# Kernel tuning notes

Measured on AMD Instinct MI355X. Metric: run time of the kernel, lower is better.

## Reference

```python
import jax, jax.numpy as jnp
import numpy as np

NUM_HEADS = 8
MODEL_DIM = 1024
SEQ_LEN = 2048


def setup_inputs() -> dict:
    key = jax.random.key(0)
    ks = jax.random.split(key, 9)
    H, D, L = NUM_HEADS, MODEL_DIM, SEQ_LEN
    s_in = 1.0 / np.sqrt(D)
    s_out = 1.0 / np.sqrt(H * D)
    return {
        "tokens": jax.random.normal(ks[0], (D, L), dtype=jnp.float32),
        "Wq": jax.random.uniform(ks[1], (H * D, D), jnp.float32, -s_in, s_in),
        "bq": jax.random.uniform(ks[2], (H * D,), jnp.float32, -s_in, s_in),
        "Wk": jax.random.uniform(ks[3], (H * D, D), jnp.float32, -s_in, s_in),
        "bk": jax.random.uniform(ks[4], (H * D,), jnp.float32, -s_in, s_in),
        "Wv": jax.random.uniform(ks[5], (H * D, D), jnp.float32, -s_in, s_in),
        "bv": jax.random.uniform(ks[6], (H * D,), jnp.float32, -s_in, s_in),
        "Wo": jax.random.uniform(ks[7], (D, H * D), jnp.float32, -s_out, s_out),
        "bo": jax.random.uniform(ks[8], (D,), jnp.float32, -s_out, s_out),
    }


def _split_heads(x, H, D, L):
    # Faithful to torch: raw .view of contiguous [H*D, L] into (L, H, D),
    # then permute(1, 2, 0) -> (H, D, L). This is a memory reinterpretation,
    # not a transpose, exactly as in the original module.
    return x.reshape(L, H, D).transpose(1, 2, 0)


def reference(tokens, Wq, bq, Wk, bk, Wv, bv, Wo, bo):
    D, L = tokens.shape
    H = Wq.shape[0] // D
    # 1x1 Conv1d == matmul over channel dim
    q = _split_heads(Wq @ tokens + bq[:, None], H, D, L)  # (H, D, L)
    k = _split_heads(Wk @ tokens + bk[:, None], H, D, L)  # (H, D, L)
    v = _split_heads(Wv @ tokens + bv[:, None], H, D, L)  # (H, D, L)
    scores = jnp.einsum("hdl,hdm->hlm", q, k) / np.sqrt(D)  # (H, L, L)
    # torch F.softmax without dim on a 3D tensor -> dim=0 (head axis)
    attn = jax.nn.softmax(scores, axis=0)
    ctx = jnp.einsum("hlm,hdm->hdl", attn, v)  # (H, D, L)
    out = Wo @ ctx.reshape(H * D, L) + bo[:, None]  # (D, L)
    return out
```

## Files before the change

### kernel.cpp

```cpp
#include <hip/hip_runtime.h>

#define SEQL 2048
#define DMODEL 1024
#define HDIM 8192

typedef unsigned short bf16_t;
typedef __attribute__((ext_vector_type(8))) short bf16x8;
typedef __attribute__((ext_vector_type(4))) float f32x4;

__device__ __forceinline__ bf16_t f2bf(float f) {
  unsigned u = __float_as_uint(f);
  u += 0x7fffu + ((u >> 16) & 1u);
  return (bf16_t)(u >> 16);
}
__device__ __forceinline__ float bf2f(bf16_t b) {
  return __uint_as_float(((unsigned)b) << 16);
}

__global__ __launch_bounds__(256) void cvt_f32_bf16(const float* __restrict__ in,
                                                    bf16_t* __restrict__ out, int n) {
  int i = (blockIdx.x * 256 + threadIdx.x) * 4;
  if (i >= n) return;
  float4 f = *reinterpret_cast<const float4*>(in + i);
  ushort4 u;
  u.x = f2bf(f.x); u.y = f2bf(f.y); u.z = f2bf(f.z); u.w = f2bf(f.w);
  *reinterpret_cast<ushort4*>(out + i) = u;
}

__global__ __launch_bounds__(256) void cvt3_f32_bf16(const float* __restrict__ a,
                                                     const float* __restrict__ b,
                                                     const float* __restrict__ c,
                                                     bf16_t* __restrict__ out) {
  const int SEG = HDIM * DMODEL;
  int i = (blockIdx.x * 256 + threadIdx.x) * 4;
  const float* src;
  int off;
  if (i < SEG) { src = a; off = i; }
  else if (i < 2 * SEG) { src = b; off = i - SEG; }
  else { src = c; off = i - 2 * SEG; }
  float4 f = *reinterpret_cast<const float4*>(src + off);
  ushort4 u;
  u.x = f2bf(f.x); u.y = f2bf(f.y); u.z = f2bf(f.z); u.w = f2bf(f.w);
  *reinterpret_cast<ushort4*>(out + i) = u;
}

__global__ __launch_bounds__(256) void bias3(const float* __restrict__ a,
                                             const float* __restrict__ b,
                                             const float* __restrict__ c,
                                             float* __restrict__ out) {
  int i = blockIdx.x * 256 + threadIdx.x;
  float v = (i < HDIM) ? a[i] : (i < 2 * HDIM) ? b[i - HDIM] : c[i - 2 * HDIM];
  out[i] = v;
}

__global__ __launch_bounds__(256) void transpose_cvt(const float* __restrict__ in,
                                                     bf16_t* __restrict__ out) {
  __shared__ float tile[32][33];
  int bx = blockIdx.x * 32;
  int by = blockIdx.y * 32;
  int tx = threadIdx.x, ty = threadIdx.y;
#pragma unroll
  for (int i = ty; i < 32; i += 8)
    tile[i][tx] = in[(size_t)(by + i) * SEQL + bx + tx];
  __syncthreads();
#pragma unroll
  for (int i = ty; i < 32; i += 8)
    out[(size_t)(bx + i) * DMODEL + by + tx] = f2bf(tile[tx][i]);
}

__global__ __launch_bounds__(256) void softmax_heads(bf16_t* __restrict__ S) {
  const size_t HS = (size_t)SEQL * SEQL;
  size_t p = ((size_t)blockIdx.x * 256 + threadIdx.x) * 8;
  float v[8][8];
#pragma unroll
  for (int h = 0; h < 8; ++h) {
    bf16x8 x = *reinterpret_cast<const bf16x8*>(S + h * HS + p);
#pragma unroll
    for (int e = 0; e < 8; ++e) v[h][e] = bf2f((bf16_t)x[e]);
  }
#pragma unroll
  for (int e = 0; e < 8; ++e) {
    float mx = v[0][e];
#pragma unroll
    for (int h = 1; h < 8; ++h) mx = fmaxf(mx, v[h][e]);
    float s = 0.f;
#pragma unroll
    for (int h = 0; h < 8; ++h) { v[h][e] = __expf(v[h][e] - mx); s += v[h][e]; }
    float inv = 1.0f / s;
#pragma unroll
    for (int h = 0; h < 8; ++h) v[h][e] *= inv;
  }
#pragma unroll
  for (int h = 0; h < 8; ++h) {
    bf16x8 x;
#pragma unroll
    for (int e = 0; e < 8; ++e) x[e] = (short)f2bf(v[h][e]);
    *reinterpret_cast<bf16x8*>(S + h * HS + p) = x;
  }
}

__global__ __launch_bounds__(256) void reduce_out(const bf16_t* __restrict__ P,
                                                  const float* __restrict__ bo,
                                                  float* __restrict__ out) {
  const size_t NEL = (size_t)DMODEL * SEQL;
  size_t i = ((size_t)blockIdx.x * 256 + threadIdx.x) * 8;
  float s[8] = {0.f, 0.f, 0.f, 0.f, 0.f, 0.f, 0.f, 0.f};
#pragma unroll
  for (int z = 0; z < 8; ++z) {
    bf16x8 x = *reinterpret_cast<const bf16x8*>(P + z * NEL + i);
#pragma unroll
    for (int e = 0; e < 8; ++e) s[e] += bf2f((bf16_t)x[e]);
  }
  float bias = bo[i >> 11];
  float4 o0 = {s[0] + bias, s[1] + bias, s[2] + bias, s[3] + bias};
  float4 o1 = {s[4] + bias, s[5] + bias, s[6] + bias, s[7] + bias};
  *reinterpret_cast<float4*>(out + i) = o0;
  *reinterpret_cast<float4*>(out + i + 4) = o1;
}

template <int EPI, bool HAS_BIAS>
__global__ __launch_bounds__(512, 2) void gemm256(
    const bf16_t* __restrict__ A, const bf16_t* __restrict__ B,
    bf16_t* __restrict__ C, bf16_t* __restrict__ C2, const float* __restrict__ bias,
    int K, int lda, int ldb, int ldc,
    long long sA, long long sB, long long sC, float scale, int gx, int gxy) {
  __shared__ alignas(16) char smem[163840];
  auto* As = reinterpret_cast<bf16_t(*)[2][8192]>(smem);
  auto* Bs = reinterpret_cast<bf16_t(*)[2][8192]>(smem + 98304);
  const int nwg = gridDim.x;
  const int bid = blockIdx.x;
  const int swz = (nwg & 7) ? bid : ((bid & 7) * (nwg >> 3) + (bid >> 3));
  const int zz = swz / gxy;
  const int rem = swz - zz * gxy;
  const int brow = (rem / gx) * 256;
  const int bcol = (rem % gx) * 256;
  A += (long long)zz * sA;
  B += (long long)zz * sB;
  C += (long long)zz * sC;
  const int tid = threadIdx.x;
  const int w = tid >> 6, lane = tid & 63;
  const int fr = lane & 15, fq = lane >> 4;
  const int wr = w >> 2, wc = w & 3;

  int rj[2], cj[2];
#pragma unroll
  for (int j = 0; j < 2; ++j) {
    const int c = (w * 2 + j) * 64 + lane;
    rj[j] = c >> 3;
    cj[j] = ((c & 7) ^ (rj[j] & 7)) << 3;
  }

  auto stageA = [&](int buf, int kk) {
#pragma unroll
    for (int half = 0; half < 2; ++half)
#pragma unroll
      for (int j = 0; j < 2; ++j) {
        const bf16_t* g = A + (size_t)(brow + half * 128 + rj[j]) * lda + kk + cj[j];
        __builtin_amdgcn_global_load_lds(
            (const __attribute__((address_space(1))) void*)g,
            (__attribute__((address_space(3))) void*)(&As[buf][half][(w * 2 + j) * 512]),
            16, 0, 0);
      }
  };
  auto stageB = [&](int buf, int kk) {
#pragma unroll
    for (int half = 0; half < 2; ++half)
#pragma unroll
      for (int j = 0; j < 2; ++j) {
        const bf16_t* g = B + (size_t)(bcol + half * 128 + rj[j]) * ldb + kk + cj[j];
        __builtin_amdgcn_global_load_lds(
            (const __attribute__((address_space(1))) void*)g,
            (__attribute__((address_space(3))) void*)(&Bs[buf][half][(w * 2 + j) * 512]),
            16, 0, 0);
      }
  };

  auto ldA = [&](int buf, int mf, int kk) -> bf16x8 {
    const int rr = mf * 16 + fr;
    return *reinterpret_cast<const bf16x8*>(
        &As[buf][wr][rr * 64 + ((((kk << 2) | fq) ^ (rr & 7)) << 3)]);
  };
  auto ldB = [&](int buf, int nf, int kk) -> bf16x8 {
    const int rr = (wc & 1) * 64 + nf * 16 + fr;
    return *reinterpret_cast<const bf16x8*>(
        &Bs[buf][wc >> 1][rr * 64 + ((((kk << 2) | fq) ^ (rr & 7)) << 3)]);
  };

  f32x4 acc[8][4];
  const f32x4 fzero = {0.f, 0.f, 0.f, 0.f};
#pragma unroll
  for (int m = 0; m < 8; ++m)
#pragma unroll
    for (int n = 0; n < 4; ++n) acc[m][n] = fzero;

  const int NT = K >> 6;

  stageA(0, 0);
  stageB(0, 0);
  stageA(1, 64);
  asm volatile("s_waitcnt vmcnt(4)" ::: "memory");
  __builtin_amdgcn_sched_barrier(0);
  __builtin_amdgcn_s_barrier();
  __builtin_amdgcn_sched_barrier(0);

  int pa = 0;
  for (int t = 0; t < NT; ++t) {
    const int pb = t & 1;
    const bool pre1 = (t + 1 < NT), pre2 = (t + 2 < NT);
    int sa = pa + 2; if (sa >= 3) sa -= 3;
    bf16x8 af[4][2], bg[4][2];

    if (pre1) stageB(pb ^ 1, (t + 1) << 6);
#pragma unroll
    for (int mf = 0; mf < 4; ++mf)
#pragma unroll
      for (int kk = 0; kk < 2; ++kk) af[mf][kk] = ldA(pa, mf, kk);
#pragma unroll
    for (int nf = 0; nf < 2; ++nf)
#pragma unroll
      for (int kk = 0; kk < 2; ++kk) bg[nf][kk] = ldB(pb, nf, kk);
    __builtin_amdgcn_s_setprio(1);
#pragma unroll
    for (int mf = 0; mf < 4; ++mf)
#pragma unroll
      for (int nf = 0; nf < 2; ++nf)
#pragma unroll
        for (int kk = 0; kk < 2; ++kk)
          acc[mf][nf] = __builtin_amdgcn_mfma_f32_16x16x32_bf16(
              af[mf][kk], bg[nf][kk], acc[mf][nf], 0, 0, 0);
    __builtin_amdgcn_s_setprio(0);

    if (pre2) stageA(sa, (t + 2) << 6);
#pragma unroll
    for (int nf = 2; nf < 4; ++nf)
#pragma unroll
      for (int kk = 0; kk < 2; ++kk) bg[nf][kk] = ldB(pb, nf, kk);
    __builtin_amdgcn_s_setprio(1);
#pragma unroll
    for (int mf = 0; mf < 4; ++mf)
#pragma unroll
      for (int nf = 2; nf < 4; ++nf)
#pragma unroll
        for (int kk = 0; kk < 2; ++kk)
          acc[mf][nf] = __builtin_amdgcn_mfma_f32_16x16x32_bf16(
              af[mf][kk], bg[nf][kk], acc[mf][nf], 0, 0, 0);
    __builtin_amdgcn_s_setprio(0);

#pragma unroll
    for (int mf = 0; mf < 4; ++mf)
#pragma unroll
      for (int kk = 0; kk < 2; ++kk) af[mf][kk] = ldA(pa, mf + 4, kk);
    __builtin_amdgcn_s_setprio(1);
#pragma unroll
    for (int mf = 0; mf < 4; ++mf)
#pragma unroll
      for (int nf = 2; nf < 4; ++nf)
#pragma unroll
        for (int kk = 0; kk < 2; ++kk)
          acc[mf + 4][nf] = __builtin_amdgcn_mfma_f32_16x16x32_bf16(
              af[mf][kk], bg[nf][kk], acc[mf + 4][nf], 0, 0, 0);
    __builtin_amdgcn_s_setprio(0);

#pragma unroll
    for (int nf = 0; nf < 2; ++nf)
#pragma unroll
      for (int kk = 0; kk < 2; ++kk) bg[nf][kk] = ldB(pb, nf, kk);
    __builtin_amdgcn_s_setprio(1);
#pragma unroll
    for (int mf = 0; mf < 4; ++mf)
#pragma unroll
      for (int nf = 0; nf < 2; ++nf)
#pragma unroll
        for (int kk = 0; kk < 2; ++kk)
          acc[mf + 4][nf] = __builtin_amdgcn_mfma_f32_16x16x32_bf16(
              af[mf][kk], bg[nf][kk], acc[mf + 4][nf], 0, 0, 0);
    __builtin_amdgcn_s_setprio(0);

    if (pre1) {
      __builtin_amdgcn_sched_barrier(0);
      if (pre2) {
        asm volatile("s_waitcnt vmcnt(4)" ::: "memory");
      } else {
        asm volatile("s_waitcnt vmcnt(0)" ::: "memory");
      }
      __builtin_amdgcn_sched_barrier(0);
      __builtin_amdgcn_s_barrier();
      __builtin_amdgcn_sched_barrier(0);
    }
    ++pa; if (pa >= 3) pa = 0;
  }

  __syncthreads();

  const bool vseg = (EPI == 2) && (brow >= 2 * HDIM);
  if ((EPI == 0) || ((EPI == 2) && !vseg)) {
    bf16_t* Ct = (bf16_t*)smem;
#pragma unroll
    for (int mf = 0; mf < 8; ++mf)
#pragma unroll
      for (int j = 0; j < 4; ++j) {
        const int orow = wr * 128 + mf * 16 + fq * 4 + j;
        float bvv = HAS_BIAS ? bias[brow + orow] : 0.f;
#pragma unroll
        for (int nf = 0; nf < 4; ++nf)
          Ct[orow * 264 + wc * 64 + nf * 16 + fr] = f2bf(acc[mf][nf][j] * scale + bvv);
      }
    __syncthreads();
#pragma unroll
    for (int i = 0; i < 16; ++i) {
      const int c = tid + i * 512;
      const int row = c >> 5, ch = c & 31;
      *reinterpret_cast<bf16x8*>(&C[(size_t)(brow + row) * ldc + bcol + ch * 8]) =
          *reinterpret_cast<const bf16x8*>(smem + row * 528 + ch * 16);
    }
  } else if constexpr (EPI == 2) {
    const int vrow = brow - 2 * HDIM;
    bf16_t* Vt = (bf16_t*)smem;
#pragma unroll
    for (int mf = 0; mf < 8; ++mf)
#pragma unroll
      for (int j = 0; j < 4; ++j) {
        const int i = wr * 128 + mf * 16 + fq * 4 + j;
        const int mloc = i >> 2;
        float bvv = HAS_BIAS ? bias[brow + i] : 0.f;
#pragma unroll
        for (int nf = 0; nf < 4; ++nf) {
          const int dloc = wc * 64 + nf * 16 + fr;
          Vt[(j * 256 + dloc) * 72 + mloc] = f2bf(acc[mf][nf][j] * scale + bvv);
        }
      }
    __syncthreads();
    const int r_ = bcol >> 10, d0 = bcol & 1023, m0 = vrow >> 2;
#pragma unroll
    for (int sIt = 0; sIt < 2; ++sIt) {
      const int s = tid + sIt * 512;
      const int h2 = s >> 8, dloc = s & 255;
      const bf16_t* src = Vt + (h2 * 256 + dloc) * 72;
      bf16_t* dst = C2 + ((size_t)(2 * h2 + r_) * DMODEL + d0 + dloc) * SEQL + m0;
#pragma unroll
      for (int qq = 0; qq < 8; ++qq)
        *reinterpret_cast<bf16x8*>(dst + qq * 8) =
            *reinterpret_cast<const bf16x8*>(src + qq * 8);
    }
  }
}

extern "C" void kernel_launch(void* const* d_in, const int* in_sizes, int n_in,
                              void* d_out, int out_size, void* d_ws, size_t ws_size,
                              hipStream_t stream) {
  const float* tokens = (const float*)d_in[0];
  const float* Wq = (const float*)d_in[1];
  const float* bq = (const float*)d_in[2];
  const float* Wk = (const float*)d_in[3];
  const float* bk = (const float*)d_in[4];
  const float* Wv = (const float*)d_in[5];
  const float* bv = (const float*)d_in[6];
  const float* Wo = (const float*)d_in[7];
  const float* bo = (const float*)d_in[8];
  float* out = (float*)d_out;
  char* ws = (char*)d_ws;
  const size_t MB = 1024ull * 1024ull;
  bf16_t* Vs = (bf16_t*)(ws + 0);
  bf16_t* QmKm = (bf16_t*)(ws + 32 * MB);
  bf16_t* Qm = QmKm;
  bf16_t* Km = QmKm + (size_t)HDIM * SEQL;
  bf16_t* Sb = (bf16_t*)(ws + 96 * MB);
  bf16_t* tT = (bf16_t*)(ws + 96 * MB);
  bf16_t* Wqkv = (bf16_t*)(ws + 100 * MB);
  float* bqkv = (float*)(ws + 148 * MB);
  bf16_t* cT = (bf16_t*)(ws + 32 * MB);
  bf16_t* Wob = (bf16_t*)(ws + 64 * MB);
  bf16_t* Pp = (bf16_t*)(ws + 96 * MB);

  dim3 b256(256);
  dim3 b512(512);
  const int nW = HDIM * DMODEL;

  transpose_cvt<<<dim3(SEQL / 32, DMODEL / 32), dim3(32, 8), 0, stream>>>(tokens, tT);
  cvt3_f32_bf16<<<3 * nW / 1024, b256, 0, stream>>>(Wq, Wk, Wv, Wqkv);
  bias3<<<3 * HDIM / 256, b256, 0, stream>>>(bq, bk, bv, bqkv);

  gemm256<2, true><<<dim3(768, 1, 1), b512, 0, stream>>>(
      Wqkv, tT, QmKm, Vs, bqkv, DMODEL, DMODEL, DMODEL, SEQL,
      0, 0, 0, 1.0f, 8, 768);

  gemm256<0, false><<<dim3(512, 1, 1), b512, 0, stream>>>(
      Qm, Km, Sb, nullptr, nullptr, DMODEL, HDIM, HDIM, SEQL,
      1024, 1024, (long long)SEQL * SEQL, 0.03125f, 8, 64);

  softmax_heads<<<(SEQL * SEQL / 8) / 256, b256, 0, stream>>>(Sb);

  gemm256<0, false><<<dim3(256, 1, 1), b512, 0, stream>>>(
      Sb, Vs, cT, nullptr, nullptr, SEQL, SEQL, SEQL, HDIM,
      (long long)SEQL * SEQL, (long long)DMODEL * SEQL, 1024, 1.0f, 4, 32);

  cvt_f32_bf16<<<nW / 1024, b256, 0, stream>>>(Wo, Wob, nW);
  gemm256<0, false><<<dim3(256, 1, 1), b512, 0, stream>>>(
      Wob, cT, Pp, nullptr, nullptr, 1024, HDIM, HDIM, SEQL,
      1024, 1024, (long long)DMODEL * SEQL, 1.0f, 8, 32);
  reduce_out<<<(DMODEL * SEQL / 8) / 256, b256, 0, stream>>>(Pp, bo, out);
}
```

Measured before the change: 357.9 us.

## Double-buffer A in GEMM main loop with per-phase barriers; hoist Wo conversion

The GEMM main loop drops the triple-buffered A tiles for double buffering, which shrinks LDS from 160 KB to 144 KB. Each MFMA phase is now wrapped in block barriers plus an lgkmcnt wait, and the A prefetch for tile t+2 moves to the last phase so it can safely overwrite the current buffer. The Wo fp32-to-bf16 conversion is launched at the start, with a new workspace location so it no longer aliases other buffers. The extra barriers per iteration add synchronisation cost and less prefetch slack, in exchange for lower LDS use and tighter lockstep scheduling across waves.

```diff
diff --git a/kernel.cpp b/kernel.cpp
--- a/kernel.cpp
+++ b/kernel.cpp
@@ -124,9 +124,9 @@
     bf16_t* __restrict__ C, bf16_t* __restrict__ C2, const float* __restrict__ bias,
     int K, int lda, int ldb, int ldc,
     long long sA, long long sB, long long sC, float scale, int gx, int gxy) {
-  __shared__ alignas(16) char smem[163840];
+  __shared__ alignas(16) char smem[147456];
   auto* As = reinterpret_cast<bf16_t(*)[2][8192]>(smem);
-  auto* Bs = reinterpret_cast<bf16_t(*)[2][8192]>(smem + 98304);
+  auto* Bs = reinterpret_cast<bf16_t(*)[2][8192]>(smem + 65536);
   const int nwg = gridDim.x;
   const int bid = blockIdx.x;
   const int swz = (nwg & 7) ? bid : ((bid & 7) * (nwg >> 3) + (bid >> 3));
@@ -186,6 +186,16 @@
         &Bs[buf][wc >> 1][rr * 64 + ((((kk << 2) | fq) ^ (rr & 7)) << 3)]);
   };
 
+#define PHASE_SYNC()                                   \
+  __builtin_amdgcn_s_barrier();                        \
+  __builtin_amdgcn_sched_barrier(0);                   \
+  asm volatile("s_waitcnt lgkmcnt(0)" ::: "memory");   \
+  __builtin_amdgcn_sched_barrier(0)
+
+#define PHASE_END()                                    \
+  __builtin_amdgcn_s_barrier();                        \
+  __builtin_amdgcn_sched_barrier(0)
+
   f32x4 acc[8][4];
   const f32x4 fzero = {0.f, 0.f, 0.f, 0.f};
 #pragma unroll
@@ -203,22 +213,21 @@
   __builtin_amdgcn_s_barrier();
   __builtin_amdgcn_sched_barrier(0);
 
-  int pa = 0;
   for (int t = 0; t < NT; ++t) {
-    const int pb = t & 1;
+    const int p = t & 1, q = p ^ 1;
     const bool pre1 = (t + 1 < NT), pre2 = (t + 2 < NT);
-    int sa = pa + 2; if (sa >= 3) sa -= 3;
     bf16x8 af[4][2], bg[4][2];
 
-    if (pre1) stageB(pb ^ 1, (t + 1) << 6);
-#pragma unroll
-    for (int mf = 0; mf < 4; ++mf)
-#pragma unroll
-      for (int kk = 0; kk < 2; ++kk) af[mf][kk] = ldA(pa, mf, kk);
+    if (pre1) stageB(q, (t + 1) << 6);
+#pragma unroll
+    for (int mf = 0; mf < 4; ++mf)
+#pragma unroll
+      for (int kk = 0; kk < 2; ++kk) af[mf][kk] = ldA(p, mf, kk);
 #pragma unroll
     for (int nf = 0; nf < 2; ++nf)
 #pragma unroll
-      for (int kk = 0; kk < 2; ++kk) bg[nf][kk] = ldB(pb, nf, kk);
+      for (int kk = 0; kk < 2; ++kk) bg[nf][kk] = ldB(p, nf, kk);
+    PHASE_SYNC();
     __builtin_amdgcn_s_setprio(1);
 #pragma unroll
     for (int mf = 0; mf < 4; ++mf)
@@ -229,12 +238,13 @@
           acc[mf][nf] = __builtin_amdgcn_mfma_f32_16x16x32_bf16(
               af[mf][kk], bg[nf][kk], acc[mf][nf], 0, 0, 0);
     __builtin_amdgcn_s_setprio(0);
-
-    if (pre2) stageA(sa, (t + 2) << 6);
+    PHASE_END();
+
 #pragma unroll
     for (int nf = 2; nf < 4; ++nf)
 #pragma unroll
-      for (int kk = 0; kk < 2; ++kk) bg[nf][kk] = ldB(pb, nf, kk);
+      for (int kk = 0; kk < 2; ++kk) bg[nf][kk] = ldB(p, nf, kk);
+    PHASE_SYNC();
     __builtin_amdgcn_s_setprio(1);
 #pragma unroll
     for (int mf = 0; mf < 4; ++mf)
@@ -245,11 +255,13 @@
           acc[mf][nf] = __builtin_amdgcn_mfma_f32_16x16x32_bf16(
               af[mf][kk], bg[nf][kk], acc[mf][nf], 0, 0, 0);
     __builtin_amdgcn_s_setprio(0);
-
-#pragma unroll
-    for (int mf = 0; mf < 4; ++mf)
-#pragma unroll
-      for (int kk = 0; kk < 2; ++kk) af[mf][kk] = ldA(pa, mf + 4, kk);
+    PHASE_END();
+
+#pragma unroll
+    for (int mf = 0; mf < 4; ++mf)
+#pragma unroll
+      for (int kk = 0; kk < 2; ++kk) af[mf][kk] = ldA(p, mf + 4, kk);
+    PHASE_SYNC();
     __builtin_amdgcn_s_setprio(1);
 #pragma unroll
     for (int mf = 0; mf < 4; ++mf)
@@ -260,11 +272,14 @@
           acc[mf + 4][nf] = __builtin_amdgcn_mfma_f32_16x16x32_bf16(
               af[mf][kk], bg[nf][kk], acc[mf + 4][nf], 0, 0, 0);
     __builtin_amdgcn_s_setprio(0);
-
+    PHASE_END();
+
+    if (pre2) stageA(p, (t + 2) << 6);
 #pragma unroll
     for (int nf = 0; nf < 2; ++nf)
 #pragma unroll
-      for (int kk = 0; kk < 2; ++kk) bg[nf][kk] = ldB(pb, nf, kk);
+      for (int kk = 0; kk < 2; ++kk) bg[nf][kk] = ldB(p, nf, kk);
+    PHASE_SYNC();
     __builtin_amdgcn_s_setprio(1);
 #pragma unroll
     for (int mf = 0; mf < 4; ++mf)
@@ -287,8 +302,9 @@
       __builtin_amdgcn_s_barrier();
       __builtin_amdgcn_sched_barrier(0);
     }
-    ++pa; if (pa >= 3) pa = 0;
-  }
+  }
+#undef PHASE_SYNC
+#undef PHASE_END
 
   __syncthreads();
 
@@ -368,8 +384,8 @@
   bf16_t* tT = (bf16_t*)(ws + 96 * MB);
   bf16_t* Wqkv = (bf16_t*)(ws + 100 * MB);
   float* bqkv = (float*)(ws + 148 * MB);
+  bf16_t* Wob = (bf16_t*)(ws + 160 * MB);
   bf16_t* cT = (bf16_t*)(ws + 32 * MB);
-  bf16_t* Wob = (bf16_t*)(ws + 64 * MB);
   bf16_t* Pp = (bf16_t*)(ws + 96 * MB);
 
   dim3 b256(256);
@@ -379,6 +395,7 @@
   transpose_cvt<<<dim3(SEQL / 32, DMODEL / 32), dim3(32, 8), 0, stream>>>(tokens, tT);
   cvt3_f32_bf16<<<3 * nW / 1024, b256, 0, stream>>>(Wq, Wk, Wv, Wqkv);
   bias3<<<3 * HDIM / 256, b256, 0, stream>>>(bq, bk, bv, bqkv);
+  cvt_f32_bf16<<<nW / 1024, b256, 0, stream>>>(Wo, Wob, nW);
 
   gemm256<2, true><<<dim3(768, 1, 1), b512, 0, stream>>>(
       Wqkv, tT, QmKm, Vs, bqkv, DMODEL, DMODEL, DMODEL, SEQL,
@@ -394,7 +411,6 @@
       Sb, Vs, cT, nullptr, nullptr, SEQL, SEQL, SEQL, HDIM,
       (long long)SEQL * SEQL, (long long)DMODEL * SEQL, 1024, 1.0f, 4, 32);
 
-  cvt_f32_bf16<<<nW / 1024, b256, 0, stream>>>(Wo, Wob, nW);
   gemm256<0, false><<<dim3(256, 1, 1), b512, 0, stream>>>(
       Wob, cT, Pp, nullptr, nullptr, 1024, HDIM, HDIM, SEQL,
       1024, 1024, (long long)DMODEL * SEQL, 1.0f, 8, 32);
```

Result: slower. 370.2 us (+3.4%).
